# Performance work log

Measured on AMD Instinct MI355X. Metric: run time of the kernel, lower is better.

Reference implementation:

```python
import jax, jax.numpy as jnp
import numpy as np

B, F, E, H, D = 8192, 50, 64, 2, 8  # batch, fields, embed, heads, domains
HD = E // H
EPS = 1e-6


def setup_inputs() -> dict:
    key = jax.random.key(0)
    ks = jax.random.split(key, 8)
    std = 0.05  # matches nn.init.normal_(std=0.05) over ALL params (incl. layernorm)
    inputs = jax.random.normal(ks[0], (B, F, E), jnp.float32)
    domain_ids = jax.random.randint(ks[1], (B,), 1, D + 1)  # values 1..D as in torch masks
    W_Query_domains = jax.random.normal(ks[2], (D, E, E), jnp.float32) * std
    W_key = jax.random.normal(ks[3], (E, E), jnp.float32) * std
    W_Value = jax.random.normal(ks[4], (E, E), jnp.float32) * std
    W_Res = jax.random.normal(ks[5], (E, E), jnp.float32) * std
    ln_scale = jax.random.normal(ks[6], (D, E), jnp.float32) * std
    ln_bias = jax.random.normal(ks[7], (D, E), jnp.float32) * std
    return dict(inputs=inputs, domain_ids=domain_ids, W_Query_domains=W_Query_domains,
                W_key=W_key, W_Value=W_Value, W_Res=W_Res,
                ln_scale=ln_scale, ln_bias=ln_bias)


def reference(inputs, domain_ids, W_Query_domains, W_key, W_Value, W_Res, ln_scale, ln_bias):
    # Eval mode: dropouts are identity. merge='no' so shared W_Query is unused.
    b, f, e = inputs.shape
    idx = domain_ids - 1  # 0-based domain index per row

    # Shared keys/values projections
    keys = jnp.einsum('bfe,eo->bfo', inputs, W_key)
    values = jnp.einsum('bfe,eo->bfo', inputs, W_Value)

    # Per-row query weight gather (replaces the python loop over domains)
    Wq = W_Query_domains[idx]  # [B,E,E]
    querys = jnp.einsum('bfe,beo->bfo', inputs, Wq)

    # Split heads: contiguous chunks of size HD along embed dim -> [B,F,H,HD]
    q = querys.reshape(b, f, H, HD)
    k = keys.reshape(b, f, H, HD)
    v = values.reshape(b, f, H, HD)

    scores = jnp.einsum('bihd,bjhd->bhij', q, k) / np.sqrt(HD).astype(np.float32)
    attn = jax.nn.softmax(scores, axis=-1)
    out = jnp.einsum('bhij,bjhd->bihd', attn, v).reshape(b, f, e)  # head concat order matches torch

    out = out + jnp.einsum('bfe,eo->bfo', inputs, W_Res)  # residual via W_Res
    out = jax.nn.relu(out)

    # Per-domain LayerNorm (gather gamma/beta per row)
    gamma = ln_scale[idx][:, None, :]  # [B,1,E]
    beta = ln_bias[idx][:, None, :]
    mean = jnp.mean(out, axis=-1, keepdims=True)
    var = jnp.mean(jnp.square(out - mean), axis=-1, keepdims=True)
    out = (out - mean) * jax.lax.rsqrt(var + EPS) * gamma + beta
    return out
```

## Files before the change

### kernel.cpp

```cpp
#include <hip/hip_runtime.h>
#include <hip/hip_bf16.h>

#define NB    8192
#define NF    50
#define NE    64

typedef __attribute__((ext_vector_type(8))) short short8;
typedef __attribute__((ext_vector_type(4))) short short4v;
typedef __attribute__((ext_vector_type(4))) float float4v;

static constexpr float SM_C   = 0.25509667991878083f;
static constexpr float LN_EPS = 1e-6f;

#define MFMA(a, b, c) __builtin_amdgcn_mfma_f32_16x16x32_bf16((a), (b), (c), 0, 0, 0)

__device__ __forceinline__ unsigned short f2bf(float f) {
    return __bfloat16_as_ushort(__float2bfloat16(f));
}

__device__ __forceinline__ int soff(int row, int col) {
    return row * 64 + ((((col >> 3) ^ row) & 7) << 3) + (col & 7);
}

__device__ __forceinline__ void st_pack4(unsigned short* p, float4v v) {
    union { unsigned short u[4]; short4v s; } r;
    r.u[0] = f2bf(v.x); r.u[1] = f2bf(v.y); r.u[2] = f2bf(v.z); r.u[3] = f2bf(v.w);
    *(short4v*)p = r.s;
}

__device__ __forceinline__ float fexp2(float x) {
#if __has_builtin(__builtin_amdgcn_exp2f)
    return __builtin_amdgcn_exp2f(x);
#else
    float r; asm("v_exp_f32 %0, %1" : "=v"(r) : "v"(x)); return r;
#endif
}

__device__ __forceinline__ float frcp(float x) {
#if __has_builtin(__builtin_amdgcn_rcpf)
    return __builtin_amdgcn_rcpf(x);
#else
    return 1.f / x;
#endif
}

__global__ void prep_weights(const float* __restrict__ wq, const float* __restrict__ wk,
                             const float* __restrict__ wv, const float* __restrict__ wr,
                             unsigned short* __restrict__ ws) {
    int i = blockIdx.x * 256 + threadIdx.x;
    if (i >= 11 * 4096) return;
    int m = i >> 12, t = i & 4095, o = t >> 6, e = t & 63;
    int po = (o & 32) | ((o & 12) << 1) | (((o >> 4) & 1) << 2) | (o & 3);
    float v;
    if (m < 8)       v = wq[(m * 64 + e) * 64 + po];
    else if (m == 8) v = wk[e * 64 + po] * SM_C;
    else if (m == 9) v = wv[e * 64 + o];
    else             v = wr[e * 64 + o];
    ws[i] = f2bf(v);
}

__global__ __launch_bounds__(128, 4)
void mdr_mfma(const float* __restrict__ x_g, const int* __restrict__ dom_g,
              const unsigned short* __restrict__ ws,
              const float* __restrict__ gam_g, const float* __restrict__ bet_g,
              float* __restrict__ out_g) {
    __shared__ __align__(16) unsigned short L[NE * NE];

    const int tid = threadIdx.x;
    const int lm  = tid & 15;
    const int lg  = (tid >> 4) & 3;
    const int u   = tid >> 6;
    const int b   = blockIdx.x;

    const int dom = dom_g[b] - 1;
    const float* xb = x_g + (size_t)b * (NF * NE);

    #pragma unroll
    for (int it = 0; it < 8; ++it) {
        int s = tid + it * 128;
        int r = s >> 4, c4 = s & 15;
        float4v v = {0.f, 0.f, 0.f, 0.f};
        if (r < NF) v = *(const float4v*)(xb + s * 4);
        st_pack4(L + soff(r, c4 * 4), v);
    }

    short8 vw[2][2];
    {
        const unsigned short* wv = ws + 9 * 4096;
        #pragma unroll
        for (int i = 0; i < 2; ++i) {
            const int t = u + 2 * i;
            vw[i][0] = *(const short8*)(wv + (lm + 16 * t) * 64 + 8 * lg);
            vw[i][1] = *(const short8*)(wv + (lm + 16 * t) * 64 + 8 * lg + 32);
        }
    }
    __syncthreads();

    short8 xf[4][2];
    #pragma unroll
    for (int mt = 0; mt < 4; ++mt) {
        xf[mt][0] = *(const short8*)(L + soff(lm + 16 * mt, 8 * lg));
        xf[mt][1] = *(const short8*)(L + soff(lm + 16 * mt, 8 * lg + 32));
    }
    __syncthreads();

    #pragma unroll
    for (int mt = 0; mt < 4; ++mt) {
        #pragma unroll
        for (int i = 0; i < 2; ++i) {
            float4v acc = {0.f, 0.f, 0.f, 0.f};
            acc = MFMA(xf[mt][0], vw[i][0], acc);
            acc = MFMA(xf[mt][1], vw[i][1], acc);
            st_pack4(L + soff(lm + 16 * (u + 2 * i),
                              32 * (mt >> 1) + 8 * lg + 4 * (mt & 1)), acc);
        }
    }

    short8 xfw[2][2];
    #pragma unroll
    for (int k = 0; k < 2; ++k) {
        xfw[0][k] = u ? xf[1][k] : xf[0][k];
        xfw[1][k] = u ? xf[3][k] : xf[2][k];
    }

    short8 kfrag[4][2];
    {
        const unsigned short* wk = ws + 8 * 4096;
        short8 kwf[4][2];
        #pragma unroll
        for (int mt = 0; mt < 4; ++mt) {
            kwf[mt][0] = *(const short8*)(wk + (lm + 16 * mt) * 64 + 8 * lg);
            kwf[mt][1] = *(const short8*)(wk + (lm + 16 * mt) * 64 + 8 * lg + 32);
        }
        #pragma unroll
        for (int jt = 0; jt < 4; ++jt) {
            #pragma unroll
            for (int h = 0; h < 2; ++h) {
                float4v z0 = {0.f, 0.f, 0.f, 0.f}, z1 = {0.f, 0.f, 0.f, 0.f};
                z0 = MFMA(kwf[2 * h][0],     xf[jt][0], z0);
                float4v a0 = MFMA(kwf[2 * h][1],     xf[jt][1], z0);
                z1 = MFMA(kwf[2 * h + 1][0], xf[jt][0], z1);
                float4v a1 = MFMA(kwf[2 * h + 1][1], xf[jt][1], z1);
                union { unsigned short uu[8]; short8 s; } r;
                #pragma unroll
                for (int r4 = 0; r4 < 4; ++r4) {
                    r.uu[r4]     = f2bf(a0[r4]);
                    r.uu[4 + r4] = f2bf(a1[r4]);
                }
                kfrag[jt][h] = r.s;
            }
        }
    }

    short8 qfrag[2][2];
    {
        const unsigned short* wq = ws + dom * 4096;
        #pragma unroll
        for (int i = 0; i < 2; ++i)
            #pragma unroll
            for (int h = 0; h < 2; ++h) {
                float4v a0, a1;
                {
                    short8 q0 = *(const short8*)(wq + (lm + 16 * (2 * h)) * 64 + 8 * lg);
                    short8 q1 = *(const short8*)(wq + (lm + 16 * (2 * h)) * 64 + 8 * lg + 32);
                    float4v z = {0.f, 0.f, 0.f, 0.f};
                    z = MFMA(q0, xfw[i][0], z);
                    a0 = MFMA(q1, xfw[i][1], z);
                }
                {
                    short8 q0 = *(const short8*)(wq + (lm + 16 * (2 * h + 1)) * 64 + 8 * lg);
                    short8 q1 = *(const short8*)(wq + (lm + 16 * (2 * h + 1)) * 64 + 8 * lg + 32);
                    float4v z = {0.f, 0.f, 0.f, 0.f};
                    z = MFMA(q0, xfw[i][0], z);
                    a1 = MFMA(q1, xfw[i][1], z);
                }
                union { unsigned short uu[8]; short8 s; } r;
                #pragma unroll
                for (int r4 = 0; r4 < 4; ++r4) {
                    r.uu[r4]     = f2bf(a0[r4]);
                    r.uu[4 + r4] = f2bf(a1[r4]);
                }
                qfrag[i][h] = r.s;
            }
    }
    __syncthreads();

    float gm[4], bt[4];
    #pragma unroll
    for (int c = 0; c < 4; ++c) {
        gm[c] = gam_g[dom * 64 + 16 * c + lm];
        bt[c] = bet_g[dom * 64 + 16 * c + lm];
    }

    #pragma unroll
    for (int i = 0; i < 2; ++i) {
        const int t = u + 2 * i;
        short8 pa[2][2];
        #pragma unroll
        for (int h = 0; h < 2; ++h) {
            float p[4][4];
            float sum = 0.f;
            #pragma unroll
            for (int jt = 0; jt < 4; ++jt) {
                float4v z = {0.f, 0.f, 0.f, 0.f};
                float4v s = MFMA(kfrag[jt][h], qfrag[i][h], z);
                #pragma unroll
                for (int r = 0; r < 4; ++r) {
                    float e = fexp2(s[r]);
                    p[jt][r] = e; sum += e;
                }
            }
            sum += __shfl_xor(sum, 16);
            sum += __shfl_xor(sum, 32);
            sum -= 14.f;
            const float ri = frcp(sum);
            #pragma unroll
            for (int ks = 0; ks < 2; ++ks) {
                union { unsigned short uu[8]; short8 s; } r;
                #pragma unroll
                for (int r4 = 0; r4 < 4; ++r4) {
                    r.uu[r4]     = f2bf(p[2 * ks][r4] * ri);
                    r.uu[4 + r4] = f2bf(p[2 * ks + 1][r4] * ri);
                }
                pa[h][ks] = r.s;
            }
        }
        float4v oacc[4];
        #pragma unroll
        for (int c = 0; c < 4; ++c) {
            oacc[c].x = 0.f; oacc[c].y = 0.f; oacc[c].z = 0.f; oacc[c].w = 0.f;
        }
        #pragma unroll
        for (int h = 0; h < 2; ++h)
            #pragma unroll
            for (int nt2 = 0; nt2 < 2; ++nt2) {
                const int c = 2 * h + nt2;
                short8 vf0 = *(const short8*)(L + soff(16 * c + lm, 8 * lg));
                short8 vf1 = *(const short8*)(L + soff(16 * c + lm, 8 * lg + 32));
                oacc[c] = MFMA(pa[h][0], vf0, oacc[c]);
                oacc[c] = MFMA(pa[h][1], vf1, oacc[c]);
            }
        {
            const unsigned short* wr = ws + 10 * 4096;
            #pragma unroll
            for (int c = 0; c < 4; ++c) {
                short8 rw0 = *(const short8*)(wr + (lm + 16 * c) * 64 + 8 * lg);
                short8 rw1 = *(const short8*)(wr + (lm + 16 * c) * 64 + 8 * lg + 32);
                oacc[c] = MFMA(xfw[i][0], rw0, oacc[c]);
                oacc[c] = MFMA(xfw[i][1], rw1, oacc[c]);
            }
        }
        float v[4][4], s1[4], s2[4];
        #pragma unroll
        for (int r = 0; r < 4; ++r) {
            #pragma unroll
            for (int c = 0; c < 4; ++c) v[r][c] = fmaxf(oacc[c][r], 0.f);
            s1[r] = v[r][0] + v[r][1] + v[r][2] + v[r][3];
            s2[r] = v[r][0]*v[r][0] + v[r][1]*v[r][1] + v[r][2]*v[r][2] + v[r][3]*v[r][3];
        }
        #pragma unroll
        for (int msk = 1; msk < 16; msk <<= 1) {
            #pragma unroll
            for (int r = 0; r < 4; ++r) {
                s1[r] += __shfl_xor(s1[r], msk);
                s2[r] += __shfl_xor(s2[r], msk);
            }
        }
        #pragma unroll
        for (int r = 0; r < 4; ++r) {
            const float mean = s1[r] * (1.f / 64.f);
            const float var  = s2[r] * (1.f / 64.f) - mean * mean;
            const float rs   = rsqrtf(var + LN_EPS);
            const int f = 16 * t + 4 * lg + r;
            if (f < NF) {
                float* op = out_g + (size_t)b * (NF * NE) + f * 64 + lm;
                #pragma unroll
                for (int c = 0; c < 4; ++c)
                    op[16 * c] = (v[r][c] - mean) * rs * gm[c] + bt[c];
            }
        }
    }
}

extern "C" void kernel_launch(void* const* d_in, const int* in_sizes, int n_in,
                              void* d_out, int out_size, void* d_ws, size_t ws_size,
                              hipStream_t stream) {
    const float* x   = (const float*)d_in[0];
    const int*   dom = (const int*)  d_in[1];
    const float* wq  = (const float*)d_in[2];
    const float* wk  = (const float*)d_in[3];
    const float* wv  = (const float*)d_in[4];
    const float* wr  = (const float*)d_in[5];
    const float* gam = (const float*)d_in[6];
    const float* bet = (const float*)d_in[7];
    unsigned short* ws = (unsigned short*)d_ws;
    float* out = (float*)d_out;

    hipLaunchKernelGGL(prep_weights, dim3(176), dim3(256), 0, stream, wq, wk, wv, wr, ws);
    hipLaunchKernelGGL(mdr_mfma, dim3(NB), dim3(128), 0, stream,
                       x, dom, ws, gam, bet, out);
}
```

Before: 95.18 us.

## Use one wavefront per batch row and load input fragments directly from global

The attention kernel now runs a single 64-thread wavefront per batch element instead of two. Each lane loads its own input rows from global memory and converts them to bf16 in registers, so the shared-memory staging pass and the associated barriers are removed. The one wavefront now computes all four V-projection tiles, all four query tiles, and all four output row tiles. This cuts redundant K-projection work and synchronisation, but it raises per-thread register pressure and serial work per wavefront, with launch bounds changed to (64,3).

```diff
diff --git a/kernel.cpp b/kernel.cpp
--- a/kernel.cpp
+++ b/kernel.cpp
@@ -59,7 +59,7 @@
     ws[i] = f2bf(v);
 }
 
-__global__ __launch_bounds__(128, 4)
+__global__ __launch_bounds__(64, 3)
 void mdr_mfma(const float* __restrict__ x_g, const int* __restrict__ dom_g,
               const unsigned short* __restrict__ ws,
               const float* __restrict__ gam_g, const float* __restrict__ bet_g,
@@ -69,58 +69,60 @@
     const int tid = threadIdx.x;
     const int lm  = tid & 15;
     const int lg  = (tid >> 4) & 3;
-    const int u   = tid >> 6;
     const int b   = blockIdx.x;
 
     const int dom = dom_g[b] - 1;
     const float* xb = x_g + (size_t)b * (NF * NE);
 
-    #pragma unroll
-    for (int it = 0; it < 8; ++it) {
-        int s = tid + it * 128;
-        int r = s >> 4, c4 = s & 15;
-        float4v v = {0.f, 0.f, 0.f, 0.f};
-        if (r < NF) v = *(const float4v*)(xb + s * 4);
-        st_pack4(L + soff(r, c4 * 4), v);
-    }
-
-    short8 vw[2][2];
+    short8 xf[4][2];
+    {
+        float4v a[4][2][2];
+        #pragma unroll
+        for (int mt = 0; mt < 4; ++mt) {
+            const int row = lm + 16 * mt;
+            const bool ok = row < NF;
+            const float* base = xb + (ok ? row * 64 : 0) + 8 * lg;
+            #pragma unroll
+            for (int ks = 0; ks < 2; ++ks) {
+                float4v z = {0.f, 0.f, 0.f, 0.f};
+                a[mt][ks][0] = ok ? *(const float4v*)(base + 32 * ks)     : z;
+                a[mt][ks][1] = ok ? *(const float4v*)(base + 32 * ks + 4) : z;
+            }
+        }
+        #pragma unroll
+        for (int mt = 0; mt < 4; ++mt)
+            #pragma unroll
+            for (int ks = 0; ks < 2; ++ks) {
+                union { unsigned short u[8]; short8 s; } r;
+                #pragma unroll
+                for (int k = 0; k < 4; ++k) {
+                    r.u[k]     = f2bf(a[mt][ks][0][k]);
+                    r.u[4 + k] = f2bf(a[mt][ks][1][k]);
+                }
+                xf[mt][ks] = r.s;
+            }
+    }
+
     {
         const unsigned short* wv = ws + 9 * 4096;
+        short8 vw[4][2];
         #pragma unroll
         for (int i = 0; i < 2; ++i) {
-            const int t = u + 2 * i;
-            vw[i][0] = *(const short8*)(wv + (lm + 16 * t) * 64 + 8 * lg);
-            vw[i][1] = *(const short8*)(wv + (lm + 16 * t) * 64 + 8 * lg + 32);
-        }
-    }
-    __syncthreads();
-
-    short8 xf[4][2];
-    #pragma unroll
-    for (int mt = 0; mt < 4; ++mt) {
-        xf[mt][0] = *(const short8*)(L + soff(lm + 16 * mt, 8 * lg));
-        xf[mt][1] = *(const short8*)(L + soff(lm + 16 * mt, 8 * lg + 32));
-    }
-    __syncthreads();
-
-    #pragma unroll
-    for (int mt = 0; mt < 4; ++mt) {
-        #pragma unroll
-        for (int i = 0; i < 2; ++i) {
-            float4v acc = {0.f, 0.f, 0.f, 0.f};
-            acc = MFMA(xf[mt][0], vw[i][0], acc);
-            acc = MFMA(xf[mt][1], vw[i][1], acc);
-            st_pack4(L + soff(lm + 16 * (u + 2 * i),
-                              32 * (mt >> 1) + 8 * lg + 4 * (mt & 1)), acc);
-        }
-    }
-
-    short8 xfw[2][2];
-    #pragma unroll
-    for (int k = 0; k < 2; ++k) {
-        xfw[0][k] = u ? xf[1][k] : xf[0][k];
-        xfw[1][k] = u ? xf[3][k] : xf[2][k];
+            vw[2*i][0]   = *(const short8*)(wv + (lm + 16 * (2*i)) * 64 + 8 * lg);
+            vw[2*i][1]   = *(const short8*)(wv + (lm + 16 * (2*i)) * 64 + 8 * lg + 32);
+            vw[2*i+1][0] = *(const short8*)(wv + (lm + 16 * (2*i+1)) * 64 + 8 * lg);
+            vw[2*i+1][1] = *(const short8*)(wv + (lm + 16 * (2*i+1)) * 64 + 8 * lg + 32);
+        }
+        #pragma unroll
+        for (int mt = 0; mt < 4; ++mt)
+            #pragma unroll
+            for (int i = 0; i < 4; ++i) {
+                float4v acc = {0.f, 0.f, 0.f, 0.f};
+                acc = MFMA(xf[mt][0], vw[i][0], acc);
+                acc = MFMA(xf[mt][1], vw[i][1], acc);
+                st_pack4(L + soff(lm + 16 * i,
+                                  32 * (mt >> 1) + 8 * lg + 4 * (mt & 1)), acc);
+            }
     }
 
     short8 kfrag[4][2];
@@ -133,7 +135,7 @@
             kwf[mt][1] = *(const short8*)(wk + (lm + 16 * mt) * 64 + 8 * lg + 32);
         }
         #pragma unroll
-        for (int jt = 0; jt < 4; ++jt) {
+        for (int jt = 0; jt < 4; ++jt)
             #pragma unroll
             for (int h = 0; h < 2; ++h) {
                 float4v z0 = {0.f, 0.f, 0.f, 0.f}, z1 = {0.f, 0.f, 0.f, 0.f};
@@ -149,31 +151,26 @@
                 }
                 kfrag[jt][h] = r.s;
             }
-        }
-    }
-
-    short8 qfrag[2][2];
+    }
+
+    short8 qfrag[4][2];
     {
         const unsigned short* wq = ws + dom * 4096;
-        #pragma unroll
-        for (int i = 0; i < 2; ++i)
+        short8 qw[4][2];
+        #pragma unroll
+        for (int mt = 0; mt < 4; ++mt) {
+            qw[mt][0] = *(const short8*)(wq + (lm + 16 * mt) * 64 + 8 * lg);
+            qw[mt][1] = *(const short8*)(wq + (lm + 16 * mt) * 64 + 8 * lg + 32);
+        }
+        #pragma unroll
+        for (int i = 0; i < 4; ++i)
             #pragma unroll
             for (int h = 0; h < 2; ++h) {
-                float4v a0, a1;
-                {
-                    short8 q0 = *(const short8*)(wq + (lm + 16 * (2 * h)) * 64 + 8 * lg);
-                    short8 q1 = *(const short8*)(wq + (lm + 16 * (2 * h)) * 64 + 8 * lg + 32);
-                    float4v z = {0.f, 0.f, 0.f, 0.f};
-                    z = MFMA(q0, xfw[i][0], z);
-                    a0 = MFMA(q1, xfw[i][1], z);
-                }
-                {
-                    short8 q0 = *(const short8*)(wq + (lm + 16 * (2 * h + 1)) * 64 + 8 * lg);
-                    short8 q1 = *(const short8*)(wq + (lm + 16 * (2 * h + 1)) * 64 + 8 * lg + 32);
-                    float4v z = {0.f, 0.f, 0.f, 0.f};
-                    z = MFMA(q0, xfw[i][0], z);
-                    a1 = MFMA(q1, xfw[i][1], z);
-                }
+                float4v z0 = {0.f, 0.f, 0.f, 0.f}, z1 = {0.f, 0.f, 0.f, 0.f};
+                z0 = MFMA(qw[2 * h][0],     xf[i][0], z0);
+                float4v a0 = MFMA(qw[2 * h][1],     xf[i][1], z0);
+                z1 = MFMA(qw[2 * h + 1][0], xf[i][0], z1);
+                float4v a1 = MFMA(qw[2 * h + 1][1], xf[i][1], z1);
                 union { unsigned short uu[8]; short8 s; } r;
                 #pragma unroll
                 for (int r4 = 0; r4 < 4; ++r4) {
@@ -193,8 +190,7 @@
     }
 
     #pragma unroll
-    for (int i = 0; i < 2; ++i) {
-        const int t = u + 2 * i;
+    for (int i = 0; i < 4; ++i) {
         short8 pa[2][2];
         #pragma unroll
         for (int h = 0; h < 2; ++h) {
@@ -246,8 +242,8 @@
             for (int c = 0; c < 4; ++c) {
                 short8 rw0 = *(const short8*)(wr + (lm + 16 * c) * 64 + 8 * lg);
                 short8 rw1 = *(const short8*)(wr + (lm + 16 * c) * 64 + 8 * lg + 32);
-                oacc[c] = MFMA(xfw[i][0], rw0, oacc[c]);
-                oacc[c] = MFMA(xfw[i][1], rw1, oacc[c]);
+                oacc[c] = MFMA(xf[i][0], rw0, oacc[c]);
+                oacc[c] = MFMA(xf[i][1], rw1, oacc[c]);
             }
         }
         float v[4][4], s1[4], s2[4];
@@ -271,7 +267,7 @@
             const float mean = s1[r] * (1.f / 64.f);
             const float var  = s2[r] * (1.f / 64.f) - mean * mean;
             const float rs   = rsqrtf(var + LN_EPS);
-            const int f = 16 * t + 4 * lg + r;
+            const int f = 16 * i + 4 * lg + r;
             if (f < NF) {
                 float* op = out_g + (size_t)b * (NF * NE) + f * 64 + lm;
                 #pragma unroll
@@ -297,6 +293,6 @@
     float* out = (float*)d_out;
 
     hipLaunchKernelGGL(prep_weights, dim3(176), dim3(256), 0, stream, wq, wk, wv, wr, ws);
-    hipLaunchKernelGGL(mdr_mfma, dim3(NB), dim3(128), 0, stream,
+    hipLaunchKernelGGL(mdr_mfma, dim3(NB), dim3(64), 0, stream,
                        x, dom, ws, gam, bet, out);
 }
```

Result: faster. 85.81 us (-9.8%).
